# Optimization experiments

Hardware: AMD Instinct MI355X
Metric: run time of the kernel (lower is better)

Reference implementation:

```python
import jax, jax.numpy as jnp
import numpy as np

# Block structure (mirrors init_kwargs)
K = 8            # number of blocks
BLK = 1024       # per-block in/out width
TOTAL = K * BLK  # total_dim = 8192
INPUT_IDX = [(i * BLK, (i + 1) * BLK) for i in range(K)]
OUTPUT_IDX = [(((i + 1) % K) * BLK, ((i + 1) % K + 1) * BLK) for i in range(K)]
BATCH = 4096


def setup_inputs() -> dict:
    key = jax.random.key(0)
    k1, k2, k3, k4 = jax.random.split(key, 4)
    x = jax.random.normal(k1, (BATCH, TOTAL), dtype=jnp.float32)
    v = jax.random.normal(k2, (BATCH, TOTAL), dtype=jnp.float32)
    # Per-block Linear params; nn.Linear default init ~ U(-1/sqrt(in), 1/sqrt(in))
    bound = 1.0 / np.sqrt(BLK)
    W = jax.random.uniform(k3, (K, BLK, BLK), dtype=jnp.float32, minval=-bound, maxval=bound)  # [K, out, in]
    b = jax.random.uniform(k4, (K, BLK), dtype=jnp.float32, minval=-bound, maxval=bound)
    return {"x": x, "v": v, "W": W, "b": b}


def reference(x, v, W, b):
    # hidden = act(v)
    hidden = jnp.tanh(v)
    # All input blocks are a uniform partition -> batch the K small GEMMs as one grouped contraction.
    h = hidden.reshape(BATCH, K, BLK)                      # [B, K, in]
    y = jnp.einsum("bki,koi->bko", h, W) + b               # [B, K, out]
    # Scatter-accumulate each block output into its padded position, plus residual x.
    result = x
    for i, (o0, o1) in enumerate(OUTPUT_IDX):
        result = result.at[:, o0:o1].add(y[:, i])
    return result
```

## Files before the change

### kernel.cpp

```cpp
#include <hip/hip_runtime.h>
#include <hip/hip_bf16.h>
#include <stdint.h>

#define BATCH 4096
#define KGRP  8
#define BLK   1024
#define TOTAL 8192

typedef __attribute__((ext_vector_type(8))) short short8;
typedef __attribute__((ext_vector_type(4))) float f32x4;

#define AS1 __attribute__((address_space(1)))
#define AS3 __attribute__((address_space(3)))


__device__ __forceinline__ unsigned short f2bf(float f) {
    union { float f; uint32_t u; } c; c.f = f;
    uint32_t u = c.u;
    u += 0x7fffu + ((u >> 16) & 1u);
    return (unsigned short)(u >> 16);
}

__device__ __forceinline__ float fast_tanh(float x) {
    float e = __expf(2.0f * x);
    return 1.0f - 2.0f / (e + 1.0f);
}

__device__ __forceinline__ void gload16(const unsigned short* src, char* dst) {
    __builtin_amdgcn_global_load_lds((const AS1 uint32_t*)src, (AS3 uint32_t*)dst, 16, 0, 0);
}

template<int N> __device__ __forceinline__ void waitvm() {
    if constexpr (N == 0)      asm volatile("s_waitcnt vmcnt(0)" ::: "memory");
    else if constexpr (N == 2) asm volatile("s_waitcnt vmcnt(2)" ::: "memory");
    else if constexpr (N == 4) asm volatile("s_waitcnt vmcnt(4)" ::: "memory");
    else if constexpr (N == 6) asm volatile("s_waitcnt vmcnt(6)" ::: "memory");
}


__global__ void k_wcast(const float4* __restrict__ W, ushort4* __restrict__ Wb) {
    const int n4 = KGRP * BLK * BLK / 4;
    for (int i = blockIdx.x * 256 + threadIdx.x; i < n4; i += 1024 * 256) {
        float4 f = W[i];
        ushort4 o;
        o.x = f2bf(f.x); o.y = f2bf(f.y); o.z = f2bf(f.z); o.w = f2bf(f.w);
        Wb[i] = o;
    }
}


template<bool WRA, bool ISSV, bool ISSB, int W>
__device__ __forceinline__ void tile_f(int kt, char* ldsp,
                                       uint32_t aRd, uint32_t bRd, uint32_t aWr,
                                       const float* vsrc, const unsigned short* BsrcT,
                                       uint32_t sdstB,
                                       float4& vc0, float4& vc1,
                                       f32x4 (*acc)[4]) {
    const uint32_t cur = (uint32_t)(kt & 1) * 24576u;
    const uint32_t oth = cur ^ 24576u;
    const char* Lb = ldsp + cur;

    short8 bfr[4], am[2];

#pragma unroll
    for (int n = 0; n < 4; ++n)
        bfr[n] = *(const short8*)(Lb + bRd + n * 1024);
#pragma unroll
    for (int i = 0; i < 2; ++i)
        am[i] = *(const short8*)(Lb + aRd + i * 1024);
    if constexpr (WRA) {
        short8 p;
        p[0] = (short)f2bf(fast_tanh(vc0.x)); p[1] = (short)f2bf(fast_tanh(vc0.y));
        p[2] = (short)f2bf(fast_tanh(vc0.z)); p[3] = (short)f2bf(fast_tanh(vc0.w));
        p[4] = (short)f2bf(fast_tanh(vc1.x)); p[5] = (short)f2bf(fast_tanh(vc1.y));
        p[6] = (short)f2bf(fast_tanh(vc1.z)); p[7] = (short)f2bf(fast_tanh(vc1.w));
        *(short8*)(ldsp + oth + aWr) = p;
    }
    if constexpr (ISSV) {
        vc0 = *(const float4*)(vsrc + (kt + 3) * 32);
        vc1 = *(const float4*)(vsrc + (kt + 3) * 32 + 4);
    }
    __builtin_amdgcn_s_setprio(1);
#pragma unroll
    for (int i = 0; i < 2; ++i)
#pragma unroll
        for (int n = 0; n < 4; ++n)
            acc[i][n] = __builtin_amdgcn_mfma_f32_16x16x32_bf16(am[i], bfr[n], acc[i][n], 0, 0, 0);
    __builtin_amdgcn_s_setprio(0);
    __builtin_amdgcn_s_barrier();
    __builtin_amdgcn_sched_barrier(0);

#pragma unroll
    for (int i = 0; i < 2; ++i)
        am[i] = *(const short8*)(Lb + aRd + (2 + i) * 1024);
    if constexpr (ISSB) {
        gload16(BsrcT + (size_t)(kt + 2) * 32, ldsp + cur + 8192u + sdstB);
        gload16(BsrcT + (size_t)128 * BLK + (size_t)(kt + 2) * 32, ldsp + cur + 16384u + sdstB);
    }
    __builtin_amdgcn_s_setprio(1);
#pragma unroll
    for (int i = 0; i < 2; ++i)
#pragma unroll
        for (int n = 0; n < 4; ++n)
            acc[2 + i][n] = __builtin_amdgcn_mfma_f32_16x16x32_bf16(am[i], bfr[n], acc[2 + i][n], 0, 0, 0);
    __builtin_amdgcn_s_setprio(0);
    if constexpr (W >= 0) {
        asm volatile("s_waitcnt lgkmcnt(0)" ::: "memory");
        waitvm<W>();
        __builtin_amdgcn_s_barrier();
        __builtin_amdgcn_sched_barrier(0);
    }
}

__global__ __launch_bounds__(512, 4)
void k_main(const float* __restrict__ v, const unsigned short* __restrict__ Wb,
            const float* __restrict__ x, const float* __restrict__ bias,
            float* __restrict__ out) {
    __shared__ __attribute__((aligned(1024))) char lds[49152];
    char* ldsp = lds;

    const int bid   = blockIdx.x;
    const int g     = bid & 7;
    const int slot  = bid >> 3;
    const int mtile = slot >> 2;
    const int ntile = slot & 3;
    const int gout  = (g + 1) & 7;

    const int tid  = threadIdx.x;
    const int lane = tid & 63;
    const int w    = tid >> 6;
    const int wr   = w >> 2;
    const int wc   = w & 3;

    const uint32_t kc  = ((uint32_t)((lane >> 4) ^ ((lane >> 1) & 3))) << 4;
    const uint32_t aRd = (uint32_t)(wr * 64 + (lane & 15)) * 64u + kc;
    const uint32_t bRd = 8192u + (uint32_t)(wc * 64 + (lane & 15)) * 64u + kc;

    const uint32_t aWr = (uint32_t)(tid >> 2) * 64u +
                         (((uint32_t)((tid & 3) ^ ((tid >> 3) & 3))) << 4);
    const float* vsrc = v + (size_t)(mtile * 128 + (tid >> 2)) * TOTAL
                          + (size_t)g * BLK + (tid & 3) * 8;

    const int sColB = ((lane & 3) ^ ((lane >> 3) & 3)) << 3;
    const unsigned short* BsrcT = Wb + (size_t)g * BLK * BLK
                                     + (size_t)(ntile * 256 + w * 16 + (lane >> 2)) * BLK + sColB;
    const uint32_t sdstB = (uint32_t)(w << 10);

    f32x4 acc[4][4];
#pragma unroll
    for (int m = 0; m < 4; ++m)
#pragma unroll
        for (int n = 0; n < 4; ++n) acc[m][n] = (f32x4){0.f, 0.f, 0.f, 0.f};

    gload16(BsrcT, ldsp + 8192u + sdstB);
    gload16(BsrcT + (size_t)128 * BLK, ldsp + 16384u + sdstB);
    gload16(BsrcT + 32, ldsp + 24576u + 8192u + sdstB);
    gload16(BsrcT + (size_t)128 * BLK + 32, ldsp + 24576u + 16384u + sdstB);
    float4 t0a = *(const float4*)(vsrc);
    float4 t0b = *(const float4*)(vsrc + 4);
    float4 vA0 = *(const float4*)(vsrc + 32), vA1 = *(const float4*)(vsrc + 36);
    float4 vB0 = *(const float4*)(vsrc + 64), vB1 = *(const float4*)(vsrc + 68);
    {
        short8 p;
        p[0] = (short)f2bf(fast_tanh(t0a.x)); p[1] = (short)f2bf(fast_tanh(t0a.y));
        p[2] = (short)f2bf(fast_tanh(t0a.z)); p[3] = (short)f2bf(fast_tanh(t0a.w));
        p[4] = (short)f2bf(fast_tanh(t0b.x)); p[5] = (short)f2bf(fast_tanh(t0b.y));
        p[6] = (short)f2bf(fast_tanh(t0b.z)); p[7] = (short)f2bf(fast_tanh(t0b.w));
        *(short8*)(ldsp + aWr) = p;
    }
    asm volatile("s_waitcnt lgkmcnt(0)" ::: "memory");
    waitvm<6>();
    __builtin_amdgcn_s_barrier();
    __builtin_amdgcn_sched_barrier(0);

#pragma unroll 1
    for (int k2 = 0; k2 < 14; ++k2) {
        tile_f<true, true, true, 4>(2 * k2,     ldsp, aRd, bRd, aWr, vsrc, BsrcT, sdstB, vA0, vA1, acc);
        tile_f<true, true, true, 4>(2 * k2 + 1, ldsp, aRd, bRd, aWr, vsrc, BsrcT, sdstB, vB0, vB1, acc);
    }
    tile_f<true, true,  true,  4>(28, ldsp, aRd, bRd, aWr, vsrc, BsrcT, sdstB, vA0, vA1, acc);
    tile_f<true, false, true,  2>(29, ldsp, aRd, bRd, aWr, vsrc, BsrcT, sdstB, vB0, vB1, acc);
    tile_f<true, false, false, 0>(30, ldsp, aRd, bRd, aWr, vsrc, BsrcT, sdstB, vA0, vA1, acc);
    tile_f<false, false, false, -1>(31, ldsp, aRd, bRd, aWr, vsrc, BsrcT, sdstB, vB0, vB1, acc);

    __builtin_amdgcn_s_barrier();

    const int q  = lane >> 4;
    const int cl = lane & 15;
    const int row0 = mtile * 128 + wr * 64;
    const int col0 = ntile * 256 + wc * 64;
    char* eb = ldsp + (uint32_t)w * 4352u;
    const float4 bias4 = *(const float4*)&bias[g * BLK + col0 + cl * 4];

#pragma unroll
    for (int m = 0; m < 4; ++m) {
#pragma unroll
        for (int n = 0; n < 4; ++n)
#pragma unroll
            for (int j = 0; j < 4; ++j)
                *(float*)(eb + (q * 4 + j) * 272 + (n * 16 + cl) * 4) = acc[m][n][j];
        asm volatile("s_waitcnt lgkmcnt(0)" ::: "memory");
        __builtin_amdgcn_sched_barrier(0);
#pragma unroll
        for (int i = 0; i < 4; ++i) {
            f32x4 vv = *(const f32x4*)(eb + (q + 4 * i) * 272 + cl * 16);
            const int r = row0 + m * 16 + q + 4 * i;
            const size_t idx = (size_t)r * TOTAL + (size_t)gout * BLK + col0 + cl * 4;
            const float4 xv = *(const float4*)&x[idx];
            float4 o;
            o.x = xv.x + bias4.x + vv[0];
            o.y = xv.y + bias4.y + vv[1];
            o.z = xv.z + bias4.z + vv[2];
            o.w = xv.w + bias4.w + vv[3];
            *(float4*)&out[idx] = o;
        }
        asm volatile("s_waitcnt lgkmcnt(0)" ::: "memory");
        __builtin_amdgcn_sched_barrier(0);
    }
}


__global__ void k_naive(const float* __restrict__ x, const float* __restrict__ v,
                        const float* __restrict__ W, const float* __restrict__ b,
                        float* __restrict__ out) {
    __shared__ float hv[BLK];
    const int bid = blockIdx.x;
    const int quarter = bid & 3;
    const int g = (bid >> 2) & 7;
    const int row = bid >> 5;
    for (int i = threadIdx.x; i < BLK; i += 256)
        hv[i] = tanhf(v[(size_t)row * TOTAL + g * BLK + i]);
    __syncthreads();
    const int o = quarter * 256 + threadIdx.x;
    const float* wrow = W + ((size_t)g * BLK + o) * BLK;
    float s = 0.f;
    for (int i = 0; i < BLK; ++i) s += hv[i] * wrow[i];
    const size_t oi = (size_t)row * TOTAL + (size_t)((g + 1) & 7) * BLK + o;
    out[oi] = x[oi] + b[g * BLK + o] + s;
}


extern "C" void kernel_launch(void* const* d_in, const int* in_sizes, int n_in,
                              void* d_out, int out_size, void* d_ws, size_t ws_size,
                              hipStream_t stream) {
    const float* x = (const float*)d_in[0];
    const float* v = (const float*)d_in[1];
    const float* W = (const float*)d_in[2];
    const float* b = (const float*)d_in[3];
    float* out = (float*)d_out;

    const size_t needW = (size_t)KGRP * BLK * BLK * sizeof(unsigned short);

    if (ws_size >= needW) {
        unsigned short* Wb = (unsigned short*)d_ws;
        k_wcast<<<1024, 256, 0, stream>>>((const float4*)W, (ushort4*)Wb);
        k_main<<<1024, 512, 0, stream>>>(v, Wb, x, b, out);
    } else {
        k_naive<<<BATCH * KGRP * 4, 256, 0, stream>>>(x, v, W, b, out);
    }
}
```

Measured before the change: 174.5 us.

## Reshape GEMM tile to 64x512 per block with deeper v prefetch

Changes the per-block tile from 128x256 to 64x512 (8 waves along N, each covering the full 64 rows), enlarging LDS double buffers to 72 KB. The activation prefetch becomes a 3-slot float4 ring loaded four tiles ahead, and the epilogue now loads x residuals before the LDS transpose. The aim is better reuse of the weight stream per block and more latency hiding on v loads. The cost is lower occupancy from the larger LDS footprint and more redundant tanh/B traffic per output.

```diff
diff --git a/kernel.cpp b/kernel.cpp
--- a/kernel.cpp
+++ b/kernel.cpp
@@ -32,9 +32,8 @@
 
 template<int N> __device__ __forceinline__ void waitvm() {
     if constexpr (N == 0)      asm volatile("s_waitcnt vmcnt(0)" ::: "memory");
-    else if constexpr (N == 2) asm volatile("s_waitcnt vmcnt(2)" ::: "memory");
     else if constexpr (N == 4) asm volatile("s_waitcnt vmcnt(4)" ::: "memory");
-    else if constexpr (N == 6) asm volatile("s_waitcnt vmcnt(6)" ::: "memory");
+    else if constexpr (N == 5) asm volatile("s_waitcnt vmcnt(5)" ::: "memory");
 }
 
 
@@ -49,15 +48,14 @@
 }
 
 
-template<bool WRA, bool ISSV, bool ISSB, int W>
+template<int SLOT, bool WRA, bool RV, bool SB, int W>
 __device__ __forceinline__ void tile_f(int kt, char* ldsp,
                                        uint32_t aRd, uint32_t bRd, uint32_t aWr,
                                        const float* vsrc, const unsigned short* BsrcT,
-                                       uint32_t sdstB,
-                                       float4& vc0, float4& vc1,
+                                       uint32_t sdstB, float4 (&vs)[3],
                                        f32x4 (*acc)[4]) {
-    const uint32_t cur = (uint32_t)(kt & 1) * 24576u;
-    const uint32_t oth = cur ^ 24576u;
+    const uint32_t cur = (uint32_t)(kt & 1) * 36864u;
+    const uint32_t oth = cur ^ 36864u;
     const char* Lb = ldsp + cur;
 
     short8 bfr[4], am[2];
@@ -69,17 +67,14 @@
     for (int i = 0; i < 2; ++i)
         am[i] = *(const short8*)(Lb + aRd + i * 1024);
     if constexpr (WRA) {
-        short8 p;
-        p[0] = (short)f2bf(fast_tanh(vc0.x)); p[1] = (short)f2bf(fast_tanh(vc0.y));
-        p[2] = (short)f2bf(fast_tanh(vc0.z)); p[3] = (short)f2bf(fast_tanh(vc0.w));
-        p[4] = (short)f2bf(fast_tanh(vc1.x)); p[5] = (short)f2bf(fast_tanh(vc1.y));
-        p[6] = (short)f2bf(fast_tanh(vc1.z)); p[7] = (short)f2bf(fast_tanh(vc1.w));
-        *(short8*)(ldsp + oth + aWr) = p;
-    }
-    if constexpr (ISSV) {
-        vc0 = *(const float4*)(vsrc + (kt + 3) * 32);
-        vc1 = *(const float4*)(vsrc + (kt + 3) * 32 + 4);
-    }
+        const float4 vc = vs[SLOT];
+        ushort4 p;
+        p.x = f2bf(fast_tanh(vc.x)); p.y = f2bf(fast_tanh(vc.y));
+        p.z = f2bf(fast_tanh(vc.z)); p.w = f2bf(fast_tanh(vc.w));
+        *(ushort4*)(ldsp + oth + aWr) = p;
+    }
+    if constexpr (RV)
+        vs[SLOT] = *(const float4*)(vsrc + (kt + 4) * 32);
     __builtin_amdgcn_s_setprio(1);
 #pragma unroll
     for (int i = 0; i < 2; ++i)
@@ -88,14 +83,15 @@
             acc[i][n] = __builtin_amdgcn_mfma_f32_16x16x32_bf16(am[i], bfr[n], acc[i][n], 0, 0, 0);
     __builtin_amdgcn_s_setprio(0);
     __builtin_amdgcn_s_barrier();
-    __builtin_amdgcn_sched_barrier(0);
 
 #pragma unroll
     for (int i = 0; i < 2; ++i)
         am[i] = *(const short8*)(Lb + aRd + (2 + i) * 1024);
-    if constexpr (ISSB) {
-        gload16(BsrcT + (size_t)(kt + 2) * 32, ldsp + cur + 8192u + sdstB);
-        gload16(BsrcT + (size_t)128 * BLK + (size_t)(kt + 2) * 32, ldsp + cur + 16384u + sdstB);
+    if constexpr (SB) {
+#pragma unroll
+        for (int c = 0; c < 4; ++c)
+            gload16(BsrcT + (size_t)(c * 128) * BLK + (size_t)(kt + 2) * 32,
+                    ldsp + cur + 4096u + (uint32_t)c * 8192u + sdstB);
     }
     __builtin_amdgcn_s_setprio(1);
 #pragma unroll
@@ -116,34 +112,33 @@
 void k_main(const float* __restrict__ v, const unsigned short* __restrict__ Wb,
             const float* __restrict__ x, const float* __restrict__ bias,
             float* __restrict__ out) {
-    __shared__ __attribute__((aligned(1024))) char lds[49152];
+    __shared__ __attribute__((aligned(1024))) char lds[73728];
     char* ldsp = lds;
 
     const int bid   = blockIdx.x;
     const int g     = bid & 7;
     const int slot  = bid >> 3;
-    const int mtile = slot >> 2;
-    const int ntile = slot & 3;
+    const int mtile = slot >> 1;
+    const int ntile = slot & 1;
     const int gout  = (g + 1) & 7;
 
     const int tid  = threadIdx.x;
     const int lane = tid & 63;
     const int w    = tid >> 6;
-    const int wr   = w >> 2;
-    const int wc   = w & 3;
 
     const uint32_t kc  = ((uint32_t)((lane >> 4) ^ ((lane >> 1) & 3))) << 4;
-    const uint32_t aRd = (uint32_t)(wr * 64 + (lane & 15)) * 64u + kc;
-    const uint32_t bRd = 8192u + (uint32_t)(wc * 64 + (lane & 15)) * 64u + kc;
-
-    const uint32_t aWr = (uint32_t)(tid >> 2) * 64u +
-                         (((uint32_t)((tid & 3) ^ ((tid >> 3) & 3))) << 4);
-    const float* vsrc = v + (size_t)(mtile * 128 + (tid >> 2)) * TOTAL
-                          + (size_t)g * BLK + (tid & 3) * 8;
-
-    const int sColB = ((lane & 3) ^ ((lane >> 3) & 3)) << 3;
+    const uint32_t aRd = (uint32_t)(lane & 15) * 64u + kc;
+    const uint32_t bRd = 4096u + (uint32_t)(w * 64 + (lane & 15)) * 64u + kc;
+
+    const uint32_t aWr = (uint32_t)(tid >> 3) * 64u +
+                         (((uint32_t)(((tid >> 1) & 3) ^ ((tid >> 4) & 3))) << 4) +
+                         (uint32_t)(tid & 1) * 8u;
+    const float* vsrc = v + (size_t)(mtile * 64 + (tid >> 3)) * TOTAL
+                          + (size_t)g * BLK + (tid & 7) * 4;
+
+    const int sColB = ((tid & 3) ^ ((tid >> 3) & 3)) << 3;
     const unsigned short* BsrcT = Wb + (size_t)g * BLK * BLK
-                                     + (size_t)(ntile * 256 + w * 16 + (lane >> 2)) * BLK + sColB;
+                                     + (size_t)(ntile * 512 + (tid >> 2)) * BLK + sColB;
     const uint32_t sdstB = (uint32_t)(w << 10);
 
     f32x4 acc[4][4];
@@ -152,48 +147,62 @@
 #pragma unroll
         for (int n = 0; n < 4; ++n) acc[m][n] = (f32x4){0.f, 0.f, 0.f, 0.f};
 
-    gload16(BsrcT, ldsp + 8192u + sdstB);
-    gload16(BsrcT + (size_t)128 * BLK, ldsp + 16384u + sdstB);
-    gload16(BsrcT + 32, ldsp + 24576u + 8192u + sdstB);
-    gload16(BsrcT + (size_t)128 * BLK + 32, ldsp + 24576u + 16384u + sdstB);
-    float4 t0a = *(const float4*)(vsrc);
-    float4 t0b = *(const float4*)(vsrc + 4);
-    float4 vA0 = *(const float4*)(vsrc + 32), vA1 = *(const float4*)(vsrc + 36);
-    float4 vB0 = *(const float4*)(vsrc + 64), vB1 = *(const float4*)(vsrc + 68);
+    float4 vs[3];
+#pragma unroll
+    for (int c = 0; c < 4; ++c)
+        gload16(BsrcT + (size_t)(c * 128) * BLK, ldsp + 4096u + (uint32_t)c * 8192u + sdstB);
+#pragma unroll
+    for (int c = 0; c < 4; ++c)
+        gload16(BsrcT + (size_t)(c * 128) * BLK + 32, ldsp + 36864u + 4096u + (uint32_t)c * 8192u + sdstB);
     {
-        short8 p;
-        p[0] = (short)f2bf(fast_tanh(t0a.x)); p[1] = (short)f2bf(fast_tanh(t0a.y));
-        p[2] = (short)f2bf(fast_tanh(t0a.z)); p[3] = (short)f2bf(fast_tanh(t0a.w));
-        p[4] = (short)f2bf(fast_tanh(t0b.x)); p[5] = (short)f2bf(fast_tanh(t0b.y));
-        p[6] = (short)f2bf(fast_tanh(t0b.z)); p[7] = (short)f2bf(fast_tanh(t0b.w));
-        *(short8*)(ldsp + aWr) = p;
+        float4 v0 = *(const float4*)(vsrc);
+        vs[1] = *(const float4*)(vsrc + 32);
+        vs[2] = *(const float4*)(vsrc + 64);
+        vs[0] = *(const float4*)(vsrc + 96);
+        ushort4 p;
+        p.x = f2bf(fast_tanh(v0.x)); p.y = f2bf(fast_tanh(v0.y));
+        p.z = f2bf(fast_tanh(v0.z)); p.w = f2bf(fast_tanh(v0.w));
+        *(ushort4*)(ldsp + aWr) = p;
     }
     asm volatile("s_waitcnt lgkmcnt(0)" ::: "memory");
-    waitvm<6>();
+    waitvm<4>();
     __builtin_amdgcn_s_barrier();
     __builtin_amdgcn_sched_barrier(0);
 
 #pragma unroll 1
-    for (int k2 = 0; k2 < 14; ++k2) {
-        tile_f<true, true, true, 4>(2 * k2,     ldsp, aRd, bRd, aWr, vsrc, BsrcT, sdstB, vA0, vA1, acc);
-        tile_f<true, true, true, 4>(2 * k2 + 1, ldsp, aRd, bRd, aWr, vsrc, BsrcT, sdstB, vB0, vB1, acc);
-    }
-    tile_f<true, true,  true,  4>(28, ldsp, aRd, bRd, aWr, vsrc, BsrcT, sdstB, vA0, vA1, acc);
-    tile_f<true, false, true,  2>(29, ldsp, aRd, bRd, aWr, vsrc, BsrcT, sdstB, vB0, vB1, acc);
-    tile_f<true, false, false, 0>(30, ldsp, aRd, bRd, aWr, vsrc, BsrcT, sdstB, vA0, vA1, acc);
-    tile_f<false, false, false, -1>(31, ldsp, aRd, bRd, aWr, vsrc, BsrcT, sdstB, vB0, vB1, acc);
-
-    __builtin_amdgcn_s_barrier();
+    for (int it = 0; it < 4; ++it) {
+        const int base = it * 6;
+        tile_f<1, true, true, true, 5>(base + 0, ldsp, aRd, bRd, aWr, vsrc, BsrcT, sdstB, vs, acc);
+        tile_f<2, true, true, true, 5>(base + 1, ldsp, aRd, bRd, aWr, vsrc, BsrcT, sdstB, vs, acc);
+        tile_f<0, true, true, true, 5>(base + 2, ldsp, aRd, bRd, aWr, vsrc, BsrcT, sdstB, vs, acc);
+        tile_f<1, true, true, true, 5>(base + 3, ldsp, aRd, bRd, aWr, vsrc, BsrcT, sdstB, vs, acc);
+        tile_f<2, true, true, true, 5>(base + 4, ldsp, aRd, bRd, aWr, vsrc, BsrcT, sdstB, vs, acc);
+        tile_f<0, true, true, true, 5>(base + 5, ldsp, aRd, bRd, aWr, vsrc, BsrcT, sdstB, vs, acc);
+    }
+    tile_f<1, true, true, true, 5>(24, ldsp, aRd, bRd, aWr, vsrc, BsrcT, sdstB, vs, acc);
+    tile_f<2, true, true, true, 5>(25, ldsp, aRd, bRd, aWr, vsrc, BsrcT, sdstB, vs, acc);
+    tile_f<0, true, true, true, 5>(26, ldsp, aRd, bRd, aWr, vsrc, BsrcT, sdstB, vs, acc);
+    tile_f<1, true, true, true, 5>(27, ldsp, aRd, bRd, aWr, vsrc, BsrcT, sdstB, vs, acc);
+    tile_f<2, true, false, true, 4>(28, ldsp, aRd, bRd, aWr, vsrc, BsrcT, sdstB, vs, acc);
+    tile_f<0, true, false, true, 4>(29, ldsp, aRd, bRd, aWr, vsrc, BsrcT, sdstB, vs, acc);
+    tile_f<1, true, false, false, 0>(30, ldsp, aRd, bRd, aWr, vsrc, BsrcT, sdstB, vs, acc);
+    tile_f<2, false, false, false, -1>(31, ldsp, aRd, bRd, aWr, vsrc, BsrcT, sdstB, vs, acc);
 
     const int q  = lane >> 4;
     const int cl = lane & 15;
-    const int row0 = mtile * 128 + wr * 64;
-    const int col0 = ntile * 256 + wc * 64;
+    const int row0 = mtile * 64;
+    const int col0 = ntile * 512 + w * 64;
     char* eb = ldsp + (uint32_t)w * 4352u;
     const float4 bias4 = *(const float4*)&bias[g * BLK + col0 + cl * 4];
 
 #pragma unroll
     for (int m = 0; m < 4; ++m) {
+        float4 xv[4];
+#pragma unroll
+        for (int i = 0; i < 4; ++i) {
+            const int r = row0 + m * 16 + q + 4 * i;
+            xv[i] = *(const float4*)&x[(size_t)r * TOTAL + (size_t)gout * BLK + col0 + cl * 4];
+        }
 #pragma unroll
         for (int n = 0; n < 4; ++n)
 #pragma unroll
@@ -206,12 +215,11 @@
             f32x4 vv = *(const f32x4*)(eb + (q + 4 * i) * 272 + cl * 16);
             const int r = row0 + m * 16 + q + 4 * i;
             const size_t idx = (size_t)r * TOTAL + (size_t)gout * BLK + col0 + cl * 4;
-            const float4 xv = *(const float4*)&x[idx];
             float4 o;
-            o.x = xv.x + bias4.x + vv[0];
-            o.y = xv.y + bias4.y + vv[1];
-            o.z = xv.z + bias4.z + vv[2];
-            o.w = xv.w + bias4.w + vv[3];
+            o.x = xv[i].x + bias4.x + vv[0];
+            o.y = xv[i].y + bias4.y + vv[1];
+            o.z = xv[i].z + bias4.z + vv[2];
+            o.w = xv[i].w + bias4.w + vv[3];
             *(float4*)&out[idx] = o;
         }
         asm volatile("s_waitcnt lgkmcnt(0)" ::: "memory");
```

Result: slower. 255.0 us (+46.1%).
